# Kernel optimization log

Hardware: AMD Instinct MI355X
Metric: run time of the kernel (lower is better)

## Reference

```python
import jax, jax.numpy as jnp
import numpy as np

XYZ_MIN = -1.0
XYZ_MAX = 1.0
GRID = 160          # world_size per axis (num_voxels=160^3)
NRAYS = 8192
NPTS = 1048576      # ~128 samples per ray
K0_DIM = 12
POS_PE = 5
VIEW_PE = 4
WIDTH = 128
DIST = 0.005        # constant step size along ray


def _trilerp(vol, pts):
    """Trilinear sample vol [C,X,Y,Z] at world-space pts [M,3] -> [M,C]."""
    C, X, Y, Z = vol.shape
    size = jnp.array([X - 1, Y - 1, Z - 1], dtype=pts.dtype)
    u = (pts - XYZ_MIN) / (XYZ_MAX - XYZ_MIN) * size
    u = jnp.clip(u, 0.0, size)
    i0 = jnp.clip(jnp.floor(u).astype(jnp.int32),
                  0, jnp.array([X - 2, Y - 2, Z - 2], dtype=jnp.int32))
    f = u - i0.astype(u.dtype)  # [M,3] fractional part
    vf = vol.reshape(C, -1)
    out = jnp.zeros((pts.shape[0], C), dtype=vol.dtype)
    for dx in (0, 1):
        wx = f[:, 0] if dx else 1.0 - f[:, 0]
        for dy in (0, 1):
            wy = f[:, 1] if dy else 1.0 - f[:, 1]
            for dz in (0, 1):
                wz = f[:, 2] if dz else 1.0 - f[:, 2]
                idx = ((i0[:, 0] + dx) * Y + (i0[:, 1] + dy)) * Z + (i0[:, 2] + dz)
                out = out + (wx * wy * wz)[:, None] * vf[:, idx].T
    return out


def _alpha2weight(alpha, ray_id, n_rays):
    """Ragged per-ray exclusive cumprod of (1-alpha) -> (weights, alphainv_last).
    Mirrors render_utils_cuda.alpha2weight: ray_id is sorted."""
    log1ma = jnp.log1p(-jnp.clip(alpha, 0.0, 1.0 - 1e-7))
    cs = jnp.cumsum(log1ma)
    excl = cs - log1ma                         # exclusive prefix sums (global)
    start = jnp.searchsorted(ray_id, jnp.arange(n_rays))  # first sample of each ray
    seg0 = excl[jnp.clip(start, 0, alpha.shape[0] - 1)]
    T = jnp.exp(excl - seg0[ray_id])           # transmittance within each ray
    weights = alpha * T
    alphainv_last = jnp.exp(jax.ops.segment_sum(log1ma, ray_id, num_segments=n_rays))
    return weights, alphainv_last


def setup_inputs() -> dict:
    key = jax.random.key(0)
    ks = jax.random.split(key, 12)
    ray_pts = jax.random.uniform(ks[0], (NPTS, 3), minval=-0.95, maxval=0.95, dtype=jnp.float32)
    ray_id = jnp.sort(jax.random.randint(ks[1], (NPTS,), 0, NRAYS, dtype=jnp.int32))
    rays_d = jax.random.normal(ks[2], (NRAYS, 3), dtype=jnp.float32)
    rays_d = rays_d / jnp.linalg.norm(rays_d, axis=-1, keepdims=True)
    # sdf grid: cube/ball-ish init + noise (sdf_init_mode)
    lin = jnp.linspace(XYZ_MIN, XYZ_MAX, GRID)
    gx, gy, gz = jnp.meshgrid(lin, lin, lin, indexing='ij')
    sdf_vol = (jnp.sqrt(gx**2 + gy**2 + gz**2) - 0.6)[None]  # [1,X,Y,Z]
    sdf_vol = (sdf_vol + 0.01 * jax.random.normal(ks[3], sdf_vol.shape)).astype(jnp.float32)
    k0_vol = 0.1 * jax.random.normal(ks[4], (K0_DIM, GRID, GRID, GRID), dtype=jnp.float32)
    dim0 = 3 + 3 * POS_PE * 2 + 3 + 3 * VIEW_PE * 2 + K0_DIM + 3  # =75
    w0 = jax.random.normal(ks[5], (dim0, WIDTH), dtype=jnp.float32) / np.sqrt(dim0)
    b0 = jnp.zeros((WIDTH,), jnp.float32)
    w1 = jax.random.normal(ks[6], (WIDTH, WIDTH), dtype=jnp.float32) / np.sqrt(WIDTH)
    b1 = jnp.zeros((WIDTH,), jnp.float32)
    w2 = jax.random.normal(ks[7], (WIDTH, 3), dtype=jnp.float32) / np.sqrt(WIDTH)
    b2 = jnp.zeros((3,), jnp.float32)
    s_val = jnp.array(0.2, dtype=jnp.float32)
    return dict(ray_pts=ray_pts, rays_d=rays_d, sdf_vol=sdf_vol, k0_vol=k0_vol,
                w0=w0, b0=b0, w1=w1, b1=b1, w2=w2, b2=b2, s_val=s_val, ray_id=ray_id)


def reference(ray_pts, rays_d, sdf_vol, k0_vol, w0, b0, w1, b1, w2, b2, s_val, ray_id):
    M = ray_pts.shape[0]
    # --- SDF + gradient (grad_mode='interpolate': central-diff grid, trilerped) ---
    sdf = _trilerp(sdf_vol, ray_pts)[:, 0]
    h = (XYZ_MAX - XYZ_MIN) / (GRID - 1)
    vol = sdf_vol[0]
    gvol = jnp.stack([jnp.gradient(vol, axis=0),
                      jnp.gradient(vol, axis=1),
                      jnp.gradient(vol, axis=2)], 0) / h  # [3,X,Y,Z]
    grad = _trilerp(gvol, ray_pts)  # [M,3]
    gn = grad / (jnp.linalg.norm(grad, axis=-1, keepdims=True) + 1e-8)
    dirs = rays_d[ray_id]  # [M,3]
    # --- NeuS-style sdf -> alpha ---
    true_cos = jnp.sum(dirs * gn, -1)
    iter_cos = -jax.nn.relu(-true_cos)  # only front-facing contributes
    inv_s = 1.0 / s_val
    prev_cdf = jax.nn.sigmoid((sdf - iter_cos * DIST * 0.5) * inv_s)
    next_cdf = jax.nn.sigmoid((sdf + iter_cos * DIST * 0.5) * inv_s)
    alpha = jnp.clip((prev_cdf - next_cdf + 1e-5) / (prev_cdf + 1e-5), 0.0, 1.0)
    # --- ragged per-ray compositing weights ---
    weights, alphainv_last = _alpha2weight(alpha, ray_id, NRAYS)
    # --- color features + MLP ---
    k0 = _trilerp(k0_vol, ray_pts)  # [M,12]
    xyz = (ray_pts - XYZ_MIN) / (XYZ_MAX - XYZ_MIN)
    posfreq = (2.0 ** jnp.arange(POS_PE)).astype(xyz.dtype)
    xe = xyz[..., None] * posfreq
    pos_emb = jnp.concatenate([xyz, jnp.sin(xe).reshape(M, -1), jnp.cos(xe).reshape(M, -1)], -1)
    viewfreq = (2.0 ** jnp.arange(VIEW_PE)).astype(xyz.dtype)
    ve = dirs[..., None] * viewfreq
    view_emb = jnp.concatenate([dirs, jnp.sin(ve).reshape(M, -1), jnp.cos(ve).reshape(M, -1)], -1)
    feat = jnp.concatenate([k0, pos_emb, view_emb, gn], -1)  # [M,75]
    hdn = jax.nn.relu(feat @ w0 + b0)
    hdn = jax.nn.relu(hdn @ w1 + b1)
    rgb = jax.nn.sigmoid(hdn @ w2 + b2)  # [M,3]
    # --- composite per ray (white background) ---
    rgb_marched = jax.ops.segment_sum(weights[:, None] * rgb, ray_id, num_segments=NRAYS)
    rgb_marched = rgb_marched + alphainv_last[:, None]
    return rgb_marched
```

## Files before the change

kernel.cpp:

```cpp
#include <hip/hip_runtime.h>
#include <math.h>

#define GRIDN 160
#define N3 (160*160*160)
#define SX (160*160)
#define SY 160
#define DIST_C 0.005f
#define W0K 104
#define W1K 136
#define TPB 16

__device__ __forceinline__ float sigm_(float x) { return 1.f / (1.f + expf(-x)); }
__device__ __forceinline__ unsigned short f2bf(float x) {
  unsigned u = __builtin_bit_cast(unsigned, x);
  u = (u + 0x7fffu + ((u >> 16) & 1u)) >> 16;
  return (unsigned short)u;
}
__device__ __forceinline__ unsigned pk_bf16(float a, float b) {
  return (unsigned)f2bf(a) | ((unsigned)f2bf(b) << 16);
}
__device__ __forceinline__ float bf_lo(unsigned u) { return __builtin_bit_cast(float, u << 16); }
__device__ __forceinline__ float bf_hi(unsigned u) { return __builtin_bit_cast(float, u & 0xffff0000u); }
__device__ __forceinline__ unsigned short f2h(float x) {
  _Float16 h = (_Float16)x; return __builtin_bit_cast(unsigned short, h);
}
__device__ __forceinline__ float h_lo(unsigned u) {
  return (float)__builtin_bit_cast(_Float16, (unsigned short)(u & 0xffffu));
}
__device__ __forceinline__ float h_hi(unsigned u) {
  return (float)__builtin_bit_cast(_Float16, (unsigned short)(u >> 16));
}

typedef __attribute__((ext_vector_type(8))) short bf16x8;
typedef __attribute__((ext_vector_type(4))) float f32x4;
typedef __attribute__((ext_vector_type(4))) unsigned u32x4;

__global__ __launch_bounds__(256) void vox_repack_all(
    const float* __restrict__ V, const float* __restrict__ k0,
    unsigned short* __restrict__ VR) {
  int idx = blockIdx.x * 256 + threadIdx.x;
  if (idx >= N3) return;
  int z = idx % GRIDN; int t = idx / GRIDN; int y = t % GRIDN; int x = t / GRIDN;
  float v = V[idx];
  float xp = (x < 159) ? V[idx + SX] : v, xm = (x > 0) ? V[idx - SX] : v;
  float yp = (y < 159) ? V[idx + SY] : v, ym = (y > 0) ? V[idx - SY] : v;
  float zp = (z < 159) ? V[idx + 1]  : v, zm = (z > 0) ? V[idx - 1]  : v;
  float cx = (x > 0 && x < 159) ? (159.f / 4.f) : (159.f / 2.f);
  float cy = (y > 0 && y < 159) ? (159.f / 4.f) : (159.f / 2.f);
  float cz = (z > 0 && z < 159) ? (159.f / 4.f) : (159.f / 2.f);
  unsigned f0 = (unsigned)f2h(v) | ((unsigned)f2h((xp - xm) * cx) << 16);
  unsigned f1 = (unsigned)f2h((yp - ym) * cy) | ((unsigned)f2h((zp - zm) * cz) << 16);
  unsigned w[6];
#pragma unroll
  for (int j = 0; j < 6; j++) {
    float a = __builtin_nontemporal_load(k0 + (size_t)(2 * j) * N3 + idx);
    float b = __builtin_nontemporal_load(k0 + (size_t)(2 * j + 1) * N3 + idx);
    w[j] = pk_bf16(a, b);
  }
  u32x4* r = (u32x4*)(VR + (size_t)idx * 16);
  r[0] = (u32x4){f0, f1, w[0], w[1]};
  r[1] = (u32x4){w[2], w[3], w[4], w[5]};
}

__global__ __launch_bounds__(256) void vox_repack_w(
    const float* __restrict__ w0, const float* __restrict__ w1, const float* __restrict__ w2,
    unsigned short* __restrict__ W0B, unsigned short* __restrict__ W1B,
    unsigned short* __restrict__ W2B) {
  int i = blockIdx.x * 256 + threadIdx.x;
  if (i < 128 * W0K) {
    int c = i / W0K, k = i - c * W0K;
    W0B[i] = (k < 75) ? f2bf(w0[k * 128 + c]) : (unsigned short)0;
  }
  if (i < 128 * W1K) {
    int c = i / W1K, k = i - c * W1K;
    W1B[i] = (k < 128) ? f2bf(w1[k * 128 + c]) : (unsigned short)0;
  }
  if (i < 16 * W1K) {
    int c = i / W1K, k = i - c * W1K;
    W2B[i] = (k < 128 && c < 3) ? f2bf(w2[k * 3 + c]) : (unsigned short)0;
  }
}

__global__ __launch_bounds__(256) void vox_gather_kernel(
    const float* __restrict__ ray_pts, const float* __restrict__ rays_d,
    const unsigned short* __restrict__ VR,
    const float* __restrict__ s_val, const int* __restrict__ ray_id,
    float* __restrict__ alpha_out, unsigned short* __restrict__ featB, int M) {
  int i = blockIdx.x * 256 + threadIdx.x;
  if (i >= M) return;

  float px = ray_pts[3 * i + 0], py = ray_pts[3 * i + 1], pz = ray_pts[3 * i + 2];
  const float SC = 0.5f * 159.f;
  float ux = fminf(fmaxf((px + 1.f) * SC, 0.f), 159.f);
  float uy = fminf(fmaxf((py + 1.f) * SC, 0.f), 159.f);
  float uz = fminf(fmaxf((pz + 1.f) * SC, 0.f), 159.f);
  int ix = min((int)ux, 158), iy = min((int)uy, 158), iz = min((int)uz, 158);
  float fx = ux - (float)ix, fy = uy - (float)iy, fz = uz - (float)iz;
  float wx0 = 1.f - fx, wy0 = 1.f - fy, wz0 = 1.f - fz;
  float wxy[4];
  wxy[0] = wx0 * wy0; wxy[1] = wx0 * fy; wxy[2] = fx * wy0; wxy[3] = fx * fy;
  const int pairoff[4] = {0, SY, SX, SX + SY};
  int base = (ix * GRIDN + iy) * GRIDN + iz;

  u32x4 q[4][4];
#pragma unroll
  for (int t = 0; t < 4; t++) {
    const u32x4* p = (const u32x4*)(VR + (size_t)(base + pairoff[t]) * 16);
    q[t][0] = p[0]; q[t][1] = p[1]; q[t][2] = p[2]; q[t][3] = p[3];
  }

  float sdf = 0.f, gx = 0.f, gy = 0.f, gz = 0.f;
  float k[12];
#pragma unroll
  for (int j = 0; j < 12; j++) k[j] = 0.f;
#pragma unroll
  for (int t = 0; t < 4; t++) {
    float w0z = wxy[t] * wz0, w1z = wxy[t] * fz;
    sdf = fmaf(w0z, h_lo(q[t][0].x), sdf);
    gx  = fmaf(w0z, h_hi(q[t][0].x), gx);
    gy  = fmaf(w0z, h_lo(q[t][0].y), gy);
    gz  = fmaf(w0z, h_hi(q[t][0].y), gz);
    k[0]  = fmaf(w0z, bf_lo(q[t][0].z), k[0]);
    k[1]  = fmaf(w0z, bf_hi(q[t][0].z), k[1]);
    k[2]  = fmaf(w0z, bf_lo(q[t][0].w), k[2]);
    k[3]  = fmaf(w0z, bf_hi(q[t][0].w), k[3]);
    k[4]  = fmaf(w0z, bf_lo(q[t][1].x), k[4]);
    k[5]  = fmaf(w0z, bf_hi(q[t][1].x), k[5]);
    k[6]  = fmaf(w0z, bf_lo(q[t][1].y), k[6]);
    k[7]  = fmaf(w0z, bf_hi(q[t][1].y), k[7]);
    k[8]  = fmaf(w0z, bf_lo(q[t][1].z), k[8]);
    k[9]  = fmaf(w0z, bf_hi(q[t][1].z), k[9]);
    k[10] = fmaf(w0z, bf_lo(q[t][1].w), k[10]);
    k[11] = fmaf(w0z, bf_hi(q[t][1].w), k[11]);
    sdf = fmaf(w1z, h_lo(q[t][2].x), sdf);
    gx  = fmaf(w1z, h_hi(q[t][2].x), gx);
    gy  = fmaf(w1z, h_lo(q[t][2].y), gy);
    gz  = fmaf(w1z, h_hi(q[t][2].y), gz);
    k[0]  = fmaf(w1z, bf_lo(q[t][2].z), k[0]);
    k[1]  = fmaf(w1z, bf_hi(q[t][2].z), k[1]);
    k[2]  = fmaf(w1z, bf_lo(q[t][2].w), k[2]);
    k[3]  = fmaf(w1z, bf_hi(q[t][2].w), k[3]);
    k[4]  = fmaf(w1z, bf_lo(q[t][3].x), k[4]);
    k[5]  = fmaf(w1z, bf_hi(q[t][3].x), k[5]);
    k[6]  = fmaf(w1z, bf_lo(q[t][3].y), k[6]);
    k[7]  = fmaf(w1z, bf_hi(q[t][3].y), k[7]);
    k[8]  = fmaf(w1z, bf_lo(q[t][3].z), k[8]);
    k[9]  = fmaf(w1z, bf_hi(q[t][3].z), k[9]);
    k[10] = fmaf(w1z, bf_lo(q[t][3].w), k[10]);
    k[11] = fmaf(w1z, bf_hi(q[t][3].w), k[11]);
  }
  float ginv = 1.f / (sqrtf(gx * gx + gy * gy + gz * gz) + 1e-8f);
  float gnx = gx * ginv, gny = gy * ginv, gnz = gz * ginv;

  int rid = ray_id[i];
  float ddx = rays_d[3 * rid + 0], ddy = rays_d[3 * rid + 1], ddz = rays_d[3 * rid + 2];

  float true_cos = ddx * gnx + ddy * gny + ddz * gnz;
  float iter_cos = fminf(true_cos, 0.f);
  float inv_s = 1.f / s_val[0];
  float e = iter_cos * (DIST_C * 0.5f);
  float prev_cdf = sigm_((sdf - e) * inv_s);
  float next_cdf = sigm_((sdf + e) * inv_s);
  float alpha = (prev_cdf - next_cdf + 1e-5f) / (prev_cdf + 1e-5f);
  alpha_out[i] = fminf(fmaxf(alpha, 0.f), 1.f);

  float feat[75];
#pragma unroll
  for (int j = 0; j < 12; j++) feat[j] = k[j];

  float x01 = (px + 1.f) * 0.5f, y01 = (py + 1.f) * 0.5f, z01 = (pz + 1.f) * 0.5f;
  feat[12] = x01; feat[13] = y01; feat[14] = z01;
#pragma unroll
  for (int l = 0; l < 5; l++) {
    float f = (float)(1 << l), s, c;
    __sincosf(x01 * f, &s, &c); feat[15 + l] = s; feat[30 + l] = c;
    __sincosf(y01 * f, &s, &c); feat[20 + l] = s; feat[35 + l] = c;
    __sincosf(z01 * f, &s, &c); feat[25 + l] = s; feat[40 + l] = c;
  }
  feat[45] = ddx; feat[46] = ddy; feat[47] = ddz;
#pragma unroll
  for (int l = 0; l < 4; l++) {
    float f = (float)(1 << l), s, c;
    __sincosf(ddx * f, &s, &c); feat[48 + l] = s; feat[60 + l] = c;
    __sincosf(ddy * f, &s, &c); feat[52 + l] = s; feat[64 + l] = c;
    __sincosf(ddz * f, &s, &c); feat[56 + l] = s; feat[68 + l] = c;
  }
  feat[72] = gnx; feat[73] = gny; feat[74] = gnz;

  unsigned pw[48];
#pragma unroll
  for (int wv = 0; wv < 37; wv++) pw[wv] = pk_bf16(feat[2 * wv], feat[2 * wv + 1]);
  pw[37] = pk_bf16(feat[74], 0.f);
#pragma unroll
  for (int wv = 38; wv < 48; wv++) pw[wv] = 0u;
  u32x4* fb = (u32x4*)(featB + (size_t)i * 96);
#pragma unroll
  for (int q2 = 0; q2 < 12; q2++)
    fb[q2] = (u32x4){pw[4 * q2], pw[4 * q2 + 1], pw[4 * q2 + 2], pw[4 * q2 + 3]};
}

__global__ __launch_bounds__(1024, 1) void vox_mlp_kernel(
    const unsigned short* __restrict__ featB,
    const unsigned short* __restrict__ W0B, const unsigned short* __restrict__ W1B,
    const unsigned short* __restrict__ W2B,
    const float* __restrict__ b0, const float* __restrict__ b1,
    const float* __restrict__ b2, float* __restrict__ rgb, int ngroups) {
  __shared__ __align__(16) unsigned short sW0[128 * W0K];
  __shared__ __align__(16) unsigned short sW1[128 * W1K];
  __shared__ __align__(16) unsigned short sW2[16 * W1K];
  __shared__ __align__(16) unsigned short sH[16 * 16 * W1K];
  __shared__ __align__(16) float sB0[128], sB1[128], sB2[16];

  {
    const uint4* s0 = (const uint4*)W0B; uint4* d0 = (uint4*)sW0;
    for (int i = threadIdx.x; i < 128 * W0K / 8; i += 1024) d0[i] = s0[i];
    const uint4* s1 = (const uint4*)W1B; uint4* d1 = (uint4*)sW1;
    for (int i = threadIdx.x; i < 128 * W1K / 8; i += 1024) d1[i] = s1[i];
    const uint4* s2 = (const uint4*)W2B; uint4* d2 = (uint4*)sW2;
    for (int i = threadIdx.x; i < 16 * W1K / 8; i += 1024) d2[i] = s2[i];
    if (threadIdx.x < 128) { sB0[threadIdx.x] = b0[threadIdx.x]; sB1[threadIdx.x] = b1[threadIdx.x]; }
    if (threadIdx.x < 16) sB2[threadIdx.x] = (threadIdx.x < 3) ? b2[threadIdx.x] : 0.f;
  }
  __syncthreads();

  const int wid = (int)(threadIdx.x >> 6), lane = (int)(threadIdx.x & 63);
  const int l15 = lane & 15, g = lane >> 4;
  unsigned short* myH = sH + wid * (16 * W1K);

#pragma unroll 1
  for (int t = 0; t < TPB; ++t) {
    int grp = blockIdx.x * TPB + t;
    if (grp >= ngroups) break;
    const int pt0 = grp * 256 + wid * 16;

    const unsigned short* fr = featB + (size_t)(pt0 + l15) * 96 + g * 8;
    bf16x8 cb0 = __builtin_nontemporal_load((const bf16x8*)(fr));
    bf16x8 cb1 = __builtin_nontemporal_load((const bf16x8*)(fr + 32));
    bf16x8 cb2 = __builtin_nontemporal_load((const bf16x8*)(fr + 64));

    f32x4 acc1[8];
#pragma unroll
    for (int m = 0; m < 8; m++) acc1[m] = (f32x4){0.f, 0.f, 0.f, 0.f};
#pragma unroll
    for (int m = 0; m < 8; m++) {
      bf16x8 a0 = *(const bf16x8*)(sW0 + (m * 16 + l15) * W0K + g * 8);
      acc1[m] = __builtin_amdgcn_mfma_f32_16x16x32_bf16(a0, cb0, acc1[m], 0, 0, 0);
      bf16x8 a1 = *(const bf16x8*)(sW0 + (m * 16 + l15) * W0K + 32 + g * 8);
      acc1[m] = __builtin_amdgcn_mfma_f32_16x16x32_bf16(a1, cb1, acc1[m], 0, 0, 0);
      bf16x8 a2 = *(const bf16x8*)(sW0 + (m * 16 + l15) * W0K + 64 + g * 8);
      acc1[m] = __builtin_amdgcn_mfma_f32_16x16x32_bf16(a2, cb2, acc1[m], 0, 0, 0);
    }
#pragma unroll
    for (int m = 0; m < 8; m++) {
      f32x4 bias = *(const f32x4*)(sB0 + m * 16 + g * 4);
      float h0 = fmaxf(acc1[m][0] + bias[0], 0.f);
      float h1 = fmaxf(acc1[m][1] + bias[1], 0.f);
      float h2 = fmaxf(acc1[m][2] + bias[2], 0.f);
      float h3 = fmaxf(acc1[m][3] + bias[3], 0.f);
      *(uint2*)(myH + l15 * W1K + m * 16 + g * 4) = make_uint2(pk_bf16(h0, h1), pk_bf16(h2, h3));
    }

    f32x4 acc2[8];
#pragma unroll
    for (int m = 0; m < 8; m++) acc2[m] = (f32x4){0.f, 0.f, 0.f, 0.f};
    const unsigned short* hb = myH + l15 * W1K + g * 8;
#pragma unroll
    for (int ks = 0; ks < 4; ks++) {
      bf16x8 bfrag = *(const bf16x8*)(hb + ks * 32);
#pragma unroll
      for (int m = 0; m < 8; m++) {
        bf16x8 afrag = *(const bf16x8*)(sW1 + (m * 16 + l15) * W1K + ks * 32 + g * 8);
        acc2[m] = __builtin_amdgcn_mfma_f32_16x16x32_bf16(afrag, bfrag, acc2[m], 0, 0, 0);
      }
    }
#pragma unroll
    for (int m = 0; m < 8; m++) {
      f32x4 bias = *(const f32x4*)(sB1 + m * 16 + g * 4);
      float h0 = fmaxf(acc2[m][0] + bias[0], 0.f);
      float h1 = fmaxf(acc2[m][1] + bias[1], 0.f);
      float h2 = fmaxf(acc2[m][2] + bias[2], 0.f);
      float h3 = fmaxf(acc2[m][3] + bias[3], 0.f);
      *(uint2*)(myH + l15 * W1K + m * 16 + g * 4) = make_uint2(pk_bf16(h0, h1), pk_bf16(h2, h3));
    }

    f32x4 acc3 = (f32x4){0.f, 0.f, 0.f, 0.f};
#pragma unroll
    for (int ks = 0; ks < 4; ks++) {
      bf16x8 bfrag = *(const bf16x8*)(hb + ks * 32);
      bf16x8 afrag = *(const bf16x8*)(sW2 + l15 * W1K + ks * 32 + g * 8);
      acc3 = __builtin_amdgcn_mfma_f32_16x16x32_bf16(afrag, bfrag, acc3, 0, 0, 0);
    }
    if (g == 0) {
      int pt = pt0 + l15;
      rgb[pt * 3 + 0] = sigm_(acc3[0] + sB2[0]);
      rgb[pt * 3 + 1] = sigm_(acc3[1] + sB2[1]);
      rgb[pt * 3 + 2] = sigm_(acc3[2] + sB2[2]);
    }
  }
}

__global__ __launch_bounds__(256) void vox_scan_kernel(
    const float* __restrict__ alpha, const float* __restrict__ rgb,
    const int* __restrict__ ray_id, float* __restrict__ out, int M, int NR) {
  int wave = (int)((blockIdx.x * blockDim.x + threadIdx.x) >> 6);
  int lane = threadIdx.x & 63;
  if (wave >= NR) return;
  int r = wave;
  int lo = 0, hi = M;
  while (lo < hi) { int mid = (lo + hi) >> 1; if (ray_id[mid] < r) lo = mid + 1; else hi = mid; }
  int start = lo; hi = M;
  while (lo < hi) { int mid = (lo + hi) >> 1; if (ray_id[mid] < r + 1) lo = mid + 1; else hi = mid; }
  int end = lo;

  float carry = 0.f, cr = 0.f, cg = 0.f, cb = 0.f;
  for (int s = start; s < end; s += 64) {
    int idx = s + lane;
    bool valid = idx < end;
    float a = valid ? alpha[idx] : 0.f;
    float l = valid ? log1pf(-fminf(a, 1.f - 1e-7f)) : 0.f;
    float sc = l;
#pragma unroll
    for (int off = 1; off < 64; off <<= 1) {
      float t = __shfl_up(sc, (unsigned)off);
      if (lane >= off) sc += t;
    }
    if (valid) {
      float T = expf(carry + (sc - l));
      float w = a * T;
      cr = fmaf(w, rgb[3 * idx + 0], cr);
      cg = fmaf(w, rgb[3 * idx + 1], cg);
      cb = fmaf(w, rgb[3 * idx + 2], cb);
    }
    carry += __shfl(sc, 63);
  }
#pragma unroll
  for (int off = 32; off > 0; off >>= 1) {
    cr += __shfl_down(cr, (unsigned)off);
    cg += __shfl_down(cg, (unsigned)off);
    cb += __shfl_down(cb, (unsigned)off);
  }
  if (lane == 0) {
    float ail = expf(carry);
    out[3 * r + 0] = cr + ail;
    out[3 * r + 1] = cg + ail;
    out[3 * r + 2] = cb + ail;
  }
}

__global__ __launch_bounds__(256) void vox_transpose_w0(
    const float* __restrict__ w0, float* __restrict__ w0t) {
  for (int idx = threadIdx.x; idx < 128 * 80; idx += 256) {
    int j = idx / 80, k = idx - j * 80;
    w0t[idx] = (k < 75) ? w0[k * 128 + j] : 0.f;
  }
}

__global__ __launch_bounds__(256) void vox_point_kernel(
    const float* __restrict__ ray_pts, const float* __restrict__ rays_d,
    const float* __restrict__ sdf_vol, const float* __restrict__ k0_vol,
    const float* __restrict__ w0t, const float* __restrict__ b0,
    const float* __restrict__ w1, const float* __restrict__ b1,
    const float* __restrict__ w2, const float* __restrict__ b2,
    const float* __restrict__ s_val, const int* __restrict__ ray_id,
    float* __restrict__ alpha_out, float* __restrict__ rgb_out, int M) {
  int i = blockIdx.x * 256 + threadIdx.x;
  if (i >= M) return;
  float px = ray_pts[3 * i + 0], py = ray_pts[3 * i + 1], pz = ray_pts[3 * i + 2];
  const float SC = 0.5f * 159.f;
  float ux = fminf(fmaxf((px + 1.f) * SC, 0.f), 159.f);
  float uy = fminf(fmaxf((py + 1.f) * SC, 0.f), 159.f);
  float uz = fminf(fmaxf((pz + 1.f) * SC, 0.f), 159.f);
  int ix = min((int)ux, 158), iy = min((int)uy, 158), iz = min((int)uz, 158);
  float fx = ux - (float)ix, fy = uy - (float)iy, fz = uz - (float)iz;
  float wx0 = 1.f - fx, wy0 = 1.f - fy, wz0 = 1.f - fz;
  float w000 = wx0 * wy0 * wz0, w001 = wx0 * wy0 * fz;
  float w010 = wx0 * fy * wz0,  w011 = wx0 * fy * fz;
  float w100 = fx * wy0 * wz0,  w101 = fx * wy0 * fz;
  float w110 = fx * fy * wz0,   w111 = fx * fy * fz;
  int base = (ix * GRIDN + iy) * GRIDN + iz;
  const float* V = sdf_vol;
  float c000 = V[base],          c001 = V[base + 1];
  float c010 = V[base + SY],     c011 = V[base + SY + 1];
  float c100 = V[base + SX],     c101 = V[base + SX + 1];
  float c110 = V[base + SX + SY], c111 = V[base + SX + SY + 1];
  float xm00 = V[base - SX],          xm01 = V[base - SX + 1];
  float xm10 = V[base - SX + SY],     xm11 = V[base - SX + SY + 1];
  float xp00 = V[base + 2 * SX],      xp01 = V[base + 2 * SX + 1];
  float xp10 = V[base + 2 * SX + SY], xp11 = V[base + 2 * SX + SY + 1];
  float ym00 = V[base - SY],          ym01 = V[base - SY + 1];
  float ym10 = V[base + SX - SY],     ym11 = V[base + SX - SY + 1];
  float yp00 = V[base + 2 * SY],      yp01 = V[base + 2 * SY + 1];
  float yp10 = V[base + SX + 2 * SY], yp11 = V[base + SX + 2 * SY + 1];
  float zm00 = V[base - 1],           zm01 = V[base + SY - 1];
  float zm10 = V[base + SX - 1],      zm11 = V[base + SX + SY - 1];
  float zp00 = V[base + 2],           zp01 = V[base + SY + 2];
  float zp10 = V[base + SX + 2],      zp11 = V[base + SX + SY + 2];
  float sdf = w000 * c000 + w001 * c001 + w010 * c010 + w011 * c011 +
              w100 * c100 + w101 * c101 + w110 * c110 + w111 * c111;
  const float INV2H = 159.f / 4.f;
  float gx = (w000 * (c100 - xm00) + w001 * (c101 - xm01) +
              w010 * (c110 - xm10) + w011 * (c111 - xm11) +
              w100 * (xp00 - c000) + w101 * (xp01 - c001) +
              w110 * (xp10 - c010) + w111 * (xp11 - c011)) * INV2H;
  float gy = (w000 * (c010 - ym00) + w001 * (c011 - ym01) +
              w100 * (c110 - ym10) + w101 * (c111 - ym11) +
              w010 * (yp00 - c000) + w011 * (yp01 - c001) +
              w110 * (yp10 - c100) + w111 * (yp11 - c101)) * INV2H;
  float gz = (w000 * (c001 - zm00) + w010 * (c011 - zm01) +
              w100 * (c101 - zm10) + w110 * (c111 - zm11) +
              w001 * (zp00 - c000) + w011 * (zp01 - c010) +
              w101 * (zp10 - c100) + w111 * (zp11 - c110)) * INV2H;
  float ginv = 1.f / (sqrtf(gx * gx + gy * gy + gz * gz) + 1e-8f);
  float gnx = gx * ginv, gny = gy * ginv, gnz = gz * ginv;
  int rid = ray_id[i];
  float ddx = rays_d[3 * rid + 0], ddy = rays_d[3 * rid + 1], ddz = rays_d[3 * rid + 2];
  float true_cos = ddx * gnx + ddy * gny + ddz * gnz;
  float iter_cos = fminf(true_cos, 0.f);
  float inv_s = 1.f / s_val[0];
  float e = iter_cos * (DIST_C * 0.5f);
  float prev_cdf = sigm_((sdf - e) * inv_s);
  float next_cdf = sigm_((sdf + e) * inv_s);
  float alpha = fminf(fmaxf((prev_cdf - next_cdf + 1e-5f) / (prev_cdf + 1e-5f), 0.f), 1.f);
  alpha_out[i] = alpha;
  float feat[75];
  {
    const int offs[8] = {0, 1, SY, SY + 1, SX, SX + 1, SX + SY, SX + SY + 1};
    const float wts[8] = {w000, w001, w010, w011, w100, w101, w110, w111};
#pragma unroll
    for (int c = 0; c < 12; c++) {
      const float* kc = k0_vol + c * N3 + base;
      float acc = 0.f;
#pragma unroll
      for (int t = 0; t < 8; t++) acc = fmaf(wts[t], kc[offs[t]], acc);
      feat[c] = acc;
    }
  }
  float x01 = (px + 1.f) * 0.5f, y01 = (py + 1.f) * 0.5f, z01 = (pz + 1.f) * 0.5f;
  feat[12] = x01; feat[13] = y01; feat[14] = z01;
#pragma unroll
  for (int l = 0; l < 5; l++) {
    float f = (float)(1 << l), s, c;
    sincosf(x01 * f, &s, &c); feat[15 + l] = s; feat[30 + l] = c;
    sincosf(y01 * f, &s, &c); feat[20 + l] = s; feat[35 + l] = c;
    sincosf(z01 * f, &s, &c); feat[25 + l] = s; feat[40 + l] = c;
  }
  feat[45] = ddx; feat[46] = ddy; feat[47] = ddz;
#pragma unroll
  for (int l = 0; l < 4; l++) {
    float f = (float)(1 << l), s, c;
    sincosf(ddx * f, &s, &c); feat[48 + l] = s; feat[60 + l] = c;
    sincosf(ddy * f, &s, &c); feat[52 + l] = s; feat[64 + l] = c;
    sincosf(ddz * f, &s, &c); feat[56 + l] = s; feat[68 + l] = c;
  }
  feat[72] = gnx; feat[73] = gny; feat[74] = gnz;
  float rr = 0.f, rg = 0.f, rb = 0.f;
#pragma unroll 1
  for (int half = 0; half < 2; ++half) {
    float acc[64];
#pragma unroll
    for (int t = 0; t < 64; t++) acc[t] = b1[half * 64 + t];
#pragma unroll 1
    for (int j = 0; j < 128; ++j) {
      float h = b0[j];
      const float* wr = w0t + j * 80;
#pragma unroll
      for (int k = 0; k < 75; k++) h = fmaf(feat[k], wr[k], h);
      h = fmaxf(h, 0.f);
      const float* w1r = w1 + j * 128 + half * 64;
#pragma unroll
      for (int t = 0; t < 64; t++) acc[t] = fmaf(h, w1r[t], acc[t]);
    }
#pragma unroll
    for (int t = 0; t < 64; t++) {
      float h2 = fmaxf(acc[t], 0.f);
      int j2 = half * 64 + t;
      rr = fmaf(h2, w2[3 * j2 + 0], rr);
      rg = fmaf(h2, w2[3 * j2 + 1], rg);
      rb = fmaf(h2, w2[3 * j2 + 2], rb);
    }
  }
  rgb_out[3 * i + 0] = sigm_(rr + b2[0]);
  rgb_out[3 * i + 1] = sigm_(rg + b2[1]);
  rgb_out[3 * i + 2] = sigm_(rb + b2[2]);
}

extern "C" void kernel_launch(void* const* d_in, const int* in_sizes, int n_in,
                              void* d_out, int out_size, void* d_ws, size_t ws_size,
                              hipStream_t stream) {
  const float* ray_pts = (const float*)d_in[0];
  const float* rays_d  = (const float*)d_in[1];
  const float* sdf_vol = (const float*)d_in[2];
  const float* k0_vol  = (const float*)d_in[3];
  const float* w0      = (const float*)d_in[4];
  const float* b0      = (const float*)d_in[5];
  const float* w1      = (const float*)d_in[6];
  const float* b1      = (const float*)d_in[7];
  const float* w2      = (const float*)d_in[8];
  const float* b2      = (const float*)d_in[9];
  const float* s_val   = (const float*)d_in[10];
  const int*   ray_id  = (const int*)d_in[11];
  float* out = (float*)d_out;

  int M  = in_sizes[0] / 3;
  int NR = in_sizes[1] / 3;

  char* ws = (char*)d_ws;
  size_t offVR   = 0;
  size_t offFeat = offVR + (size_t)N3 * 32;
  size_t offA    = offFeat + (size_t)M * 96 * 2;
  size_t offRgb  = offA + (size_t)M * 4;
  size_t offW0   = offRgb + (size_t)M * 12;
  size_t offW1   = offW0 + (size_t)128 * W0K * 2;
  size_t offW2   = offW1 + (size_t)128 * W1K * 2;
  size_t need    = offW2 + (size_t)16 * W1K * 2;

  if (ws_size >= need && (M % 256) == 0) {
    unsigned short* VR = (unsigned short*)(ws + offVR);
    unsigned short* featB = (unsigned short*)(ws + offFeat);
    float* alpha_ws = (float*)(ws + offA);
    float* rgb_ws = (float*)(ws + offRgb);
    unsigned short* W0B = (unsigned short*)(ws + offW0);
    unsigned short* W1B = (unsigned short*)(ws + offW1);
    unsigned short* W2B = (unsigned short*)(ws + offW2);

    int ngroups = M / 256;
    vox_repack_all<<<(N3 + 255) / 256, 256, 0, stream>>>(sdf_vol, k0_vol, VR);
    vox_repack_w<<<(128 * W1K + 255) / 256, 256, 0, stream>>>(w0, w1, w2, W0B, W1B, W2B);
    vox_gather_kernel<<<(M + 255) / 256, 256, 0, stream>>>(
        ray_pts, rays_d, VR, s_val, ray_id, alpha_ws, featB, M);
    vox_mlp_kernel<<<(ngroups + TPB - 1) / TPB, 1024, 0, stream>>>(
        featB, W0B, W1B, W2B, b0, b1, b2, rgb_ws, ngroups);
    vox_scan_kernel<<<(NR * 64 + 255) / 256, 256, 0, stream>>>(
        alpha_ws, rgb_ws, ray_id, out, M, NR);
  } else {
    float* alpha_ws = (float*)ws;
    float* rgb_ws   = (float*)(ws + (size_t)M * 4);
    float* w0t_ws   = (float*)(ws + (size_t)M * 16);
    vox_transpose_w0<<<1, 256, 0, stream>>>(w0, w0t_ws);
    vox_point_kernel<<<(M + 255) / 256, 256, 0, stream>>>(
        ray_pts, rays_d, sdf_vol, k0_vol, w0t_ws, b0, w1, b1, w2, b2,
        s_val, ray_id, alpha_ws, rgb_ws, M);
    vox_scan_kernel<<<(NR * 64 + 255) / 256, 256, 0, stream>>>(
        alpha_ws, rgb_ws, ray_id, out, M, NR);
  }
}
```

Measured before the change: 345.5 us.

## Recompute positional/view encodings in MLP kernel instead of storing full features

The gather kernel now writes only the 12 trilinear k0 features plus the normalized gradient (32 bytes per point) instead of the full 192-byte padded bf16 feature vector. The MLP kernel reloads ray points, ray ids and directions and recomputes the sin/cos encodings, building each lane's MFMA B-fragment directly in registers via a per-lane-group switch. This cuts intermediate global write and read traffic but adds redundant transcendental work and register pressure to the MLP kernel. Each lane computes all encodings even though it packs only a subset.

```diff
diff --git a/kernel.cpp b/kernel.cpp
--- a/kernel.cpp
+++ b/kernel.cpp
@@ -85,7 +85,7 @@
     const float* __restrict__ ray_pts, const float* __restrict__ rays_d,
     const unsigned short* __restrict__ VR,
     const float* __restrict__ s_val, const int* __restrict__ ray_id,
-    float* __restrict__ alpha_out, unsigned short* __restrict__ featB, int M) {
+    float* __restrict__ alpha_out, unsigned short* __restrict__ TD, int M) {
   int i = blockIdx.x * 256 + threadIdx.x;
   if (i >= M) return;
 
@@ -164,43 +164,16 @@
   float alpha = (prev_cdf - next_cdf + 1e-5f) / (prev_cdf + 1e-5f);
   alpha_out[i] = fminf(fmaxf(alpha, 0.f), 1.f);
 
-  float feat[75];
-#pragma unroll
-  for (int j = 0; j < 12; j++) feat[j] = k[j];
-
-  float x01 = (px + 1.f) * 0.5f, y01 = (py + 1.f) * 0.5f, z01 = (pz + 1.f) * 0.5f;
-  feat[12] = x01; feat[13] = y01; feat[14] = z01;
-#pragma unroll
-  for (int l = 0; l < 5; l++) {
-    float f = (float)(1 << l), s, c;
-    __sincosf(x01 * f, &s, &c); feat[15 + l] = s; feat[30 + l] = c;
-    __sincosf(y01 * f, &s, &c); feat[20 + l] = s; feat[35 + l] = c;
-    __sincosf(z01 * f, &s, &c); feat[25 + l] = s; feat[40 + l] = c;
-  }
-  feat[45] = ddx; feat[46] = ddy; feat[47] = ddz;
-#pragma unroll
-  for (int l = 0; l < 4; l++) {
-    float f = (float)(1 << l), s, c;
-    __sincosf(ddx * f, &s, &c); feat[48 + l] = s; feat[60 + l] = c;
-    __sincosf(ddy * f, &s, &c); feat[52 + l] = s; feat[64 + l] = c;
-    __sincosf(ddz * f, &s, &c); feat[56 + l] = s; feat[68 + l] = c;
-  }
-  feat[72] = gnx; feat[73] = gny; feat[74] = gnz;
-
-  unsigned pw[48];
-#pragma unroll
-  for (int wv = 0; wv < 37; wv++) pw[wv] = pk_bf16(feat[2 * wv], feat[2 * wv + 1]);
-  pw[37] = pk_bf16(feat[74], 0.f);
-#pragma unroll
-  for (int wv = 38; wv < 48; wv++) pw[wv] = 0u;
-  u32x4* fb = (u32x4*)(featB + (size_t)i * 96);
-#pragma unroll
-  for (int q2 = 0; q2 < 12; q2++)
-    fb[q2] = (u32x4){pw[4 * q2], pw[4 * q2 + 1], pw[4 * q2 + 2], pw[4 * q2 + 3]};
+  u32x4* tb = (u32x4*)(TD + (size_t)i * 16);
+  tb[0] = (u32x4){pk_bf16(k[0], k[1]), pk_bf16(k[2], k[3]),
+                  pk_bf16(k[4], k[5]), pk_bf16(k[6], k[7])};
+  tb[1] = (u32x4){pk_bf16(k[8], k[9]), pk_bf16(k[10], k[11]),
+                  pk_bf16(gnx, gny), pk_bf16(gnz, 0.f)};
 }
 
 __global__ __launch_bounds__(1024, 1) void vox_mlp_kernel(
-    const unsigned short* __restrict__ featB,
+    const float* __restrict__ ray_pts, const float* __restrict__ rays_d,
+    const int* __restrict__ ray_id, const unsigned short* __restrict__ TD,
     const unsigned short* __restrict__ W0B, const unsigned short* __restrict__ W1B,
     const unsigned short* __restrict__ W2B,
     const float* __restrict__ b0, const float* __restrict__ b1,
@@ -232,11 +205,71 @@
     int grp = blockIdx.x * TPB + t;
     if (grp >= ngroups) break;
     const int pt0 = grp * 256 + wid * 16;
-
-    const unsigned short* fr = featB + (size_t)(pt0 + l15) * 96 + g * 8;
-    bf16x8 cb0 = __builtin_nontemporal_load((const bf16x8*)(fr));
-    bf16x8 cb1 = __builtin_nontemporal_load((const bf16x8*)(fr + 32));
-    bf16x8 cb2 = __builtin_nontemporal_load((const bf16x8*)(fr + 64));
+    const int pt = pt0 + l15;
+
+    float px = ray_pts[3 * pt + 0], py = ray_pts[3 * pt + 1], pz = ray_pts[3 * pt + 2];
+    int rid = ray_id[pt];
+    float ddx = rays_d[3 * rid + 0], ddy = rays_d[3 * rid + 1], ddz = rays_d[3 * rid + 2];
+    float x01 = (px + 1.f) * 0.5f, y01 = (py + 1.f) * 0.5f, z01 = (pz + 1.f) * 0.5f;
+    float snx[5], csx[5], sny[5], csy[5], snz[5], csz[5];
+    float sdx[4], cdx[4], sdy[4], cdy[4], sdz[4], cdz[4];
+#pragma unroll
+    for (int l = 0; l < 5; l++) {
+      float f = (float)(1 << l);
+      __sincosf(x01 * f, &snx[l], &csx[l]);
+      __sincosf(y01 * f, &sny[l], &csy[l]);
+      __sincosf(z01 * f, &snz[l], &csz[l]);
+    }
+#pragma unroll
+    for (int l = 0; l < 4; l++) {
+      float f = (float)(1 << l);
+      __sincosf(ddx * f, &sdx[l], &cdx[l]);
+      __sincosf(ddy * f, &sdy[l], &cdy[l]);
+      __sincosf(ddz * f, &sdz[l], &cdz[l]);
+    }
+    const u32x4* tdp = (const u32x4*)(TD + (size_t)pt * 16);
+    u32x4 td0 = tdp[0];
+    u32x4 td1 = tdp[1];
+
+    bf16x8 cb0, cb1, cb2;
+    const u32x4 zz = (u32x4){0u, 0u, 0u, 0u};
+    switch (g) {
+      case 0:
+        cb0 = __builtin_bit_cast(bf16x8, td0);
+        cb1 = __builtin_bit_cast(bf16x8, (u32x4){
+            pk_bf16(csx[2], csx[3]), pk_bf16(csx[4], csy[0]),
+            pk_bf16(csy[1], csy[2]), pk_bf16(csy[3], csy[4])});
+        cb2 = __builtin_bit_cast(bf16x8, (u32x4){
+            pk_bf16(cdy[0], cdy[1]), pk_bf16(cdy[2], cdy[3]),
+            pk_bf16(cdz[0], cdz[1]), pk_bf16(cdz[2], cdz[3])});
+        break;
+      case 1:
+        cb0 = __builtin_bit_cast(bf16x8, (u32x4){
+            td1.x, td1.y, pk_bf16(x01, y01), pk_bf16(z01, snx[0])});
+        cb1 = __builtin_bit_cast(bf16x8, (u32x4){
+            pk_bf16(csz[0], csz[1]), pk_bf16(csz[2], csz[3]),
+            pk_bf16(csz[4], ddx), pk_bf16(ddy, ddz)});
+        cb2 = __builtin_bit_cast(bf16x8, (u32x4){td1.z, td1.w, 0u, 0u});
+        break;
+      case 2:
+        cb0 = __builtin_bit_cast(bf16x8, (u32x4){
+            pk_bf16(snx[1], snx[2]), pk_bf16(snx[3], snx[4]),
+            pk_bf16(sny[0], sny[1]), pk_bf16(sny[2], sny[3])});
+        cb1 = __builtin_bit_cast(bf16x8, (u32x4){
+            pk_bf16(sdx[0], sdx[1]), pk_bf16(sdx[2], sdx[3]),
+            pk_bf16(sdy[0], sdy[1]), pk_bf16(sdy[2], sdy[3])});
+        cb2 = __builtin_bit_cast(bf16x8, zz);
+        break;
+      default:
+        cb0 = __builtin_bit_cast(bf16x8, (u32x4){
+            pk_bf16(sny[4], snz[0]), pk_bf16(snz[1], snz[2]),
+            pk_bf16(snz[3], snz[4]), pk_bf16(csx[0], csx[1])});
+        cb1 = __builtin_bit_cast(bf16x8, (u32x4){
+            pk_bf16(sdz[0], sdz[1]), pk_bf16(sdz[2], sdz[3]),
+            pk_bf16(cdx[0], cdx[1]), pk_bf16(cdx[2], cdx[3])});
+        cb2 = __builtin_bit_cast(bf16x8, zz);
+        break;
+    }
 
     f32x4 acc1[8];
 #pragma unroll
@@ -291,7 +324,6 @@
       acc3 = __builtin_amdgcn_mfma_f32_16x16x32_bf16(afrag, bfrag, acc3, 0, 0, 0);
     }
     if (g == 0) {
-      int pt = pt0 + l15;
       rgb[pt * 3 + 0] = sigm_(acc3[0] + sB2[0]);
       rgb[pt * 3 + 1] = sigm_(acc3[1] + sB2[1]);
       rgb[pt * 3 + 2] = sigm_(acc3[2] + sB2[2]);
@@ -506,8 +538,8 @@
 
   char* ws = (char*)d_ws;
   size_t offVR   = 0;
-  size_t offFeat = offVR + (size_t)N3 * 32;
-  size_t offA    = offFeat + (size_t)M * 96 * 2;
+  size_t offTD   = offVR + (size_t)N3 * 32;
+  size_t offA    = offTD + (size_t)M * 32;
   size_t offRgb  = offA + (size_t)M * 4;
   size_t offW0   = offRgb + (size_t)M * 12;
   size_t offW1   = offW0 + (size_t)128 * W0K * 2;
@@ -516,7 +548,7 @@
 
   if (ws_size >= need && (M % 256) == 0) {
     unsigned short* VR = (unsigned short*)(ws + offVR);
-    unsigned short* featB = (unsigned short*)(ws + offFeat);
+    unsigned short* TD = (unsigned short*)(ws + offTD);
     float* alpha_ws = (float*)(ws + offA);
     float* rgb_ws = (float*)(ws + offRgb);
     unsigned short* W0B = (unsigned short*)(ws + offW0);
@@ -527,9 +559,9 @@
     vox_repack_all<<<(N3 + 255) / 256, 256, 0, stream>>>(sdf_vol, k0_vol, VR);
     vox_repack_w<<<(128 * W1K + 255) / 256, 256, 0, stream>>>(w0, w1, w2, W0B, W1B, W2B);
     vox_gather_kernel<<<(M + 255) / 256, 256, 0, stream>>>(
-        ray_pts, rays_d, VR, s_val, ray_id, alpha_ws, featB, M);
+        ray_pts, rays_d, VR, s_val, ray_id, alpha_ws, TD, M);
     vox_mlp_kernel<<<(ngroups + TPB - 1) / TPB, 1024, 0, stream>>>(
-        featB, W0B, W1B, W2B, b0, b1, b2, rgb_ws, ngroups);
+        ray_pts, rays_d, ray_id, TD, W0B, W1B, W2B, b0, b1, b2, rgb_ws, ngroups);
     vox_scan_kernel<<<(NR * 64 + 255) / 256, 256, 0, stream>>>(
         alpha_ws, rgb_ws, ray_id, out, M, NR);
   } else {
```

Result: faster. 316.6 us (-8.4%).
